# Optimization experiments

Hardware: AMD Instinct MI355X
Metric: run time of the kernel (lower is better)

Reference implementation:

```python
import jax, jax.numpy as jnp
import numpy as np

OVERFLOW_MARGIN = 1e-08

N, D, OUT = 8192, 128, 128


def setup_inputs() -> dict:
    key = jax.random.key(0)
    k1, k2, k3 = jax.random.split(key, 3)
    values = jax.random.normal(k1, (N, D), dtype=jnp.float32)
    adjacency = jax.random.uniform(k2, (N, N), dtype=jnp.float32)
    W = jax.random.normal(k3, (D, OUT), dtype=jnp.float32) * 0.05
    b = jnp.zeros((OUT,), dtype=jnp.float32)
    return {"values": values, "adjacency": adjacency, "W": W, "b": b}


def reference(values, adjacency, W, b):
    # Dense projection: fc_sc = values @ W + b  -> [N, OUT]
    fc_sc = values @ W + b
    # degree d = A @ ones -> row sums, [N]
    d = jnp.sum(adjacency, axis=1)
    d_inv_sqrt = 1.0 / (jnp.sqrt(d) + OVERFLOW_MARGIN)  # [N]
    # laplacian = diag(d_inv_sqrt) @ A @ diag(d_inv_sqrt)
    # expressed as row/col broadcast scaling (same math, no NxN diag matmuls)
    laplacian = adjacency * d_inv_sqrt[:, None] * d_inv_sqrt[None, :]
    # graph conv: [N,N] @ [N,OUT]
    return laplacian @ fc_sc
```

## Files before the change

### kernel.cpp

```cpp
#include <hip/hip_runtime.h>

#define NROWS 8192
#define DIM   128
#define RS    132

typedef __attribute__((ext_vector_type(8))) short  short8;
typedef __attribute__((ext_vector_type(4))) float  floatx4;

__device__ __forceinline__ unsigned pk_bf16(float a, float b) {
  unsigned ua = __float_as_uint(a);
  ua += 0x7fffu + ((ua >> 16) & 1u);
  unsigned ub = __float_as_uint(b);
  ub += 0x7fffu + ((ub >> 16) & 1u);
  return (ua >> 16) | (ub & 0xffff0000u);
}

__global__ __launch_bounds__(256) void k_rowsum(const float* __restrict__ A,
                                                float* __restrict__ d) {
  int w = threadIdx.x >> 6, lane = threadIdx.x & 63;
  int row = blockIdx.x * 4 + w;
  const float* ap = A + (size_t)row * NROWS + lane * 4;
  float sum = 0.f;
#pragma unroll
  for (int it = 0; it < 32; ++it) {
    float4 v = *(const float4*)(ap + (size_t)it * 256);
    sum += (v.x + v.y) + (v.z + v.w);
  }
#pragma unroll
  for (int off = 32; off; off >>= 1) sum += __shfl_down(sum, off, 64);
  if (lane == 0) d[row] = sum;
}

__global__ __launch_bounds__(256) void k_sconv(const float* __restrict__ d,
                                               float* __restrict__ s) {
  int i = blockIdx.x * 256 + threadIdx.x;
  s[i] = 1.0f / (sqrtf(d[i]) + 1e-8f);
}

__global__ __launch_bounds__(256) void k_fc(const float* __restrict__ V,
                                            const float* __restrict__ W,
                                            const float* __restrict__ b,
                                            const float* __restrict__ s,
                                            unsigned short* __restrict__ gTt) {
  __shared__ float Wl[DIM * DIM];
  __shared__ float Vl[32 * DIM];
  __shared__ unsigned short Fl[32 * DIM];
  int r0 = blockIdx.x * 32;
  {
    const float4* Wg = (const float4*)W;
    float4* Wd = (float4*)Wl;
#pragma unroll
    for (int i = 0; i < DIM * DIM / 4 / 256; ++i)
      Wd[threadIdx.x + i * 256] = Wg[threadIdx.x + i * 256];
    const float4* Vg = (const float4*)(V + (size_t)r0 * DIM);
    float4* Vd = (float4*)Vl;
#pragma unroll
    for (int i = 0; i < 32 * DIM / 4 / 256; ++i)
      Vd[threadIdx.x + i * 256] = Vg[threadIdx.x + i * 256];
  }
  __syncthreads();

  int cg = threadIdx.x & 31;
  int rg = threadIdx.x >> 5;
  float acc[4][4] = {};
  for (int dd = 0; dd < DIM; ++dd) {
    float4 w = *(const float4*)&Wl[dd * DIM + cg * 4];
#pragma unroll
    for (int rr = 0; rr < 4; ++rr) {
      float v = Vl[(rg * 4 + rr) * DIM + dd];
      acc[rr][0] += v * w.x; acc[rr][1] += v * w.y;
      acc[rr][2] += v * w.z; acc[rr][3] += v * w.w;
    }
  }
  float bb[4], sv[4];
#pragma unroll
  for (int cc = 0; cc < 4; ++cc) bb[cc] = b[cg * 4 + cc];
#pragma unroll
  for (int rr = 0; rr < 4; ++rr) sv[rr] = s[r0 + rg * 4 + rr];
#pragma unroll
  for (int rr = 0; rr < 4; ++rr)
#pragma unroll
    for (int cc = 0; cc < 4; cc += 2) {
      unsigned p = pk_bf16((acc[rr][cc]     + bb[cc])     * sv[rr],
                           (acc[rr][cc + 1] + bb[cc + 1]) * sv[rr]);
      *(unsigned*)&Fl[(rg * 4 + rr) * DIM + cg * 4 + cc] = p;
    }
  __syncthreads();

  int kblk = threadIdx.x >> 5, s5 = threadIdx.x & 31;
  int jblk = r0 >> 5;
#pragma unroll
  for (int h = 0; h < 2; ++h) {
    int L = s5 + h * 32;
    int l15 = L & 15, quad = L >> 4;
    int k = kblk * 16 + l15;
    unsigned w0 = (unsigned)Fl[(quad * 8 + 0) * DIM + k] | ((unsigned)Fl[(quad * 8 + 1) * DIM + k] << 16);
    unsigned w1 = (unsigned)Fl[(quad * 8 + 2) * DIM + k] | ((unsigned)Fl[(quad * 8 + 3) * DIM + k] << 16);
    unsigned w2 = (unsigned)Fl[(quad * 8 + 4) * DIM + k] | ((unsigned)Fl[(quad * 8 + 5) * DIM + k] << 16);
    unsigned w3 = (unsigned)Fl[(quad * 8 + 6) * DIM + k] | ((unsigned)Fl[(quad * 8 + 7) * DIM + k] << 16);
    *(uint4*)(gTt + ((size_t)(kblk * 256 + jblk) * 64 + L) * 8) = make_uint4(w0, w1, w2, w3);
  }
}

__global__ __launch_bounds__(256, 2) void k_spmm(const float* __restrict__ A,
                                                 const unsigned short* __restrict__ gTt,
                                                 const float* __restrict__ s,
                                                 float* __restrict__ out) {
  __shared__ float red[4 * 32 * RS];
  int t = threadIdx.x, w = t >> 6, lane = t & 63;
  int l15 = lane & 15, quad = lane >> 4;
  int bi = blockIdx.x;
  int jblk0 = w * 64;

  const float* ap0 = A + (size_t)(bi * 32 + l15) * NROWS + jblk0 * 32 + quad * 8;
  const float* ap1 = ap0 + (size_t)16 * NROWS;
  const unsigned short* gb = gTt + (size_t)jblk0 * 512 + lane * 8;

  floatx4 acc[8][2];
#pragma unroll
  for (int kb = 0; kb < 8; ++kb)
#pragma unroll
    for (int ib = 0; ib < 2; ++ib)
      acc[kb][ib] = (floatx4){0.f, 0.f, 0.f, 0.f};

#pragma unroll 2
  for (int it = 0; it < 64; ++it) {
    float4 a0lo = *(const float4*)(ap0);
    float4 a0hi = *(const float4*)(ap0 + 4);
    float4 a1lo = *(const float4*)(ap1);
    float4 a1hi = *(const float4*)(ap1 + 4);
    short8 gf[8];
#pragma unroll
    for (int kb = 0; kb < 8; ++kb)
      gf[kb] = *(const short8*)(gb + (size_t)kb * 256 * 512);
    union { unsigned u[4]; short8 s8; } c0, c1;
    c0.u[0] = pk_bf16(a0lo.x, a0lo.y); c0.u[1] = pk_bf16(a0lo.z, a0lo.w);
    c0.u[2] = pk_bf16(a0hi.x, a0hi.y); c0.u[3] = pk_bf16(a0hi.z, a0hi.w);
    c1.u[0] = pk_bf16(a1lo.x, a1lo.y); c1.u[1] = pk_bf16(a1lo.z, a1lo.w);
    c1.u[2] = pk_bf16(a1hi.x, a1hi.y); c1.u[3] = pk_bf16(a1hi.z, a1hi.w);
#pragma unroll
    for (int kb = 0; kb < 8; ++kb) {
      acc[kb][0] = __builtin_amdgcn_mfma_f32_16x16x32_bf16(gf[kb], c0.s8, acc[kb][0], 0, 0, 0);
      acc[kb][1] = __builtin_amdgcn_mfma_f32_16x16x32_bf16(gf[kb], c1.s8, acc[kb][1], 0, 0, 0);
    }
    ap0 += 32; ap1 += 32; gb += 512;
  }

  float* myred = red + w * 32 * RS;
#pragma unroll
  for (int ib = 0; ib < 2; ++ib)
#pragma unroll
    for (int kb = 0; kb < 8; ++kb) {
      float4 v = make_float4(acc[kb][ib][0], acc[kb][ib][1], acc[kb][ib][2], acc[kb][ib][3]);
      *(float4*)(myred + (ib * 16 + l15) * RS + kb * 16 + quad * 4) = v;
    }
  __syncthreads();

  int ii = t >> 3, kg = (t & 7) * 16;
  float4 sum[4];
#pragma unroll
  for (int c = 0; c < 4; ++c) sum[c] = make_float4(0.f, 0.f, 0.f, 0.f);
#pragma unroll
  for (int ww = 0; ww < 4; ++ww)
#pragma unroll
    for (int c = 0; c < 4; ++c) {
      float4 v = *(const float4*)(red + ww * 32 * RS + ii * RS + kg + c * 4);
      sum[c].x += v.x; sum[c].y += v.y; sum[c].z += v.z; sum[c].w += v.w;
    }
  float si = s[bi * 32 + ii];
  float* pout = out + ((size_t)(bi * 32 + ii)) * 128 + kg;
#pragma unroll
  for (int c = 0; c < 4; ++c) {
    float4 r = make_float4(si * sum[c].x, si * sum[c].y, si * sum[c].z, si * sum[c].w);
    *(float4*)(pout + c * 4) = r;
  }
}

extern "C" void kernel_launch(void* const* d_in, const int* in_sizes, int n_in,
                              void* d_out, int out_size, void* d_ws, size_t ws_size,
                              hipStream_t stream) {
  const float* values    = (const float*)d_in[0];
  const float* adjacency = (const float*)d_in[1];
  const float* W         = (const float*)d_in[2];
  const float* b         = (const float*)d_in[3];
  float* out = (float*)d_out;

  char* ws = (char*)d_ws;
  float* d            = (float*)ws;
  float* s            = (float*)(ws + 32768);
  unsigned short* gTt = (unsigned short*)(ws + 65536);

  k_rowsum<<<NROWS / 4, 256, 0, stream>>>(adjacency, d);
  k_sconv<<<NROWS / 256, 256, 0, stream>>>(d, s);
  k_fc<<<NROWS / 32, 256, 0, stream>>>(values, W, b, s, gTt);
  k_spmm<<<256, 256, 0, stream>>>(adjacency, gTt, s, out);
}
```

Measured before the change: 431.6 us.

## Fuse rsqrt into rowsum, widen SpMM split-K to 8 waves, use hardware bf16 pack

```diff
diff --git a/kernel.cpp b/kernel.cpp
--- a/kernel.cpp
+++ b/kernel.cpp
@@ -1,4 +1,5 @@
 #include <hip/hip_runtime.h>
+#include <hip/hip_bf16.h>
 
 #define NROWS 8192
 #define DIM   128
@@ -15,8 +16,13 @@
   return (ua >> 16) | (ub & 0xffff0000u);
 }
 
+__device__ __forceinline__ unsigned cvt_pk2(float lo, float hi) {
+  __hip_bfloat162 h = __float22bfloat162_rn(float2{lo, hi});
+  return *reinterpret_cast<unsigned*>(&h);
+}
+
 __global__ __launch_bounds__(256) void k_rowsum(const float* __restrict__ A,
-                                                float* __restrict__ d) {
+                                                float* __restrict__ s) {
   int w = threadIdx.x >> 6, lane = threadIdx.x & 63;
   int row = blockIdx.x * 4 + w;
   const float* ap = A + (size_t)row * NROWS + lane * 4;
@@ -28,13 +34,7 @@
   }
 #pragma unroll
   for (int off = 32; off; off >>= 1) sum += __shfl_down(sum, off, 64);
-  if (lane == 0) d[row] = sum;
-}
-
-__global__ __launch_bounds__(256) void k_sconv(const float* __restrict__ d,
-                                               float* __restrict__ s) {
-  int i = blockIdx.x * 256 + threadIdx.x;
-  s[i] = 1.0f / (sqrtf(d[i]) + 1e-8f);
+  if (lane == 0) s[row] = 1.0f / (sqrtf(sum) + 1e-8f);
 }
 
 __global__ __launch_bounds__(256) void k_fc(const float* __restrict__ V,
@@ -102,15 +102,15 @@
   }
 }
 
-__global__ __launch_bounds__(256, 2) void k_spmm(const float* __restrict__ A,
-                                                 const unsigned short* __restrict__ gTt,
-                                                 const float* __restrict__ s,
-                                                 float* __restrict__ out) {
-  __shared__ float red[4 * 32 * RS];
+__global__ __launch_bounds__(512) void k_spmm(const float* __restrict__ A,
+                                              const unsigned short* __restrict__ gTt,
+                                              const float* __restrict__ s,
+                                              float* __restrict__ out) {
+  __shared__ float red[8 * 32 * RS];
   int t = threadIdx.x, w = t >> 6, lane = t & 63;
   int l15 = lane & 15, quad = lane >> 4;
   int bi = blockIdx.x;
-  int jblk0 = w * 64;
+  int jblk0 = w * 32;
 
   const float* ap0 = A + (size_t)(bi * 32 + l15) * NROWS + jblk0 * 32 + quad * 8;
   const float* ap1 = ap0 + (size_t)16 * NROWS;
@@ -124,7 +124,7 @@
       acc[kb][ib] = (floatx4){0.f, 0.f, 0.f, 0.f};
 
 #pragma unroll 2
-  for (int it = 0; it < 64; ++it) {
+  for (int it = 0; it < 32; ++it) {
     float4 a0lo = *(const float4*)(ap0);
     float4 a0hi = *(const float4*)(ap0 + 4);
     float4 a1lo = *(const float4*)(ap1);
@@ -134,10 +134,10 @@
     for (int kb = 0; kb < 8; ++kb)
       gf[kb] = *(const short8*)(gb + (size_t)kb * 256 * 512);
     union { unsigned u[4]; short8 s8; } c0, c1;
-    c0.u[0] = pk_bf16(a0lo.x, a0lo.y); c0.u[1] = pk_bf16(a0lo.z, a0lo.w);
-    c0.u[2] = pk_bf16(a0hi.x, a0hi.y); c0.u[3] = pk_bf16(a0hi.z, a0hi.w);
-    c1.u[0] = pk_bf16(a1lo.x, a1lo.y); c1.u[1] = pk_bf16(a1lo.z, a1lo.w);
-    c1.u[2] = pk_bf16(a1hi.x, a1hi.y); c1.u[3] = pk_bf16(a1hi.z, a1hi.w);
+    c0.u[0] = cvt_pk2(a0lo.x, a0lo.y); c0.u[1] = cvt_pk2(a0lo.z, a0lo.w);
+    c0.u[2] = cvt_pk2(a0hi.x, a0hi.y); c0.u[3] = cvt_pk2(a0hi.z, a0hi.w);
+    c1.u[0] = cvt_pk2(a1lo.x, a1lo.y); c1.u[1] = cvt_pk2(a1lo.z, a1lo.w);
+    c1.u[2] = cvt_pk2(a1hi.x, a1hi.y); c1.u[3] = cvt_pk2(a1hi.z, a1hi.w);
 #pragma unroll
     for (int kb = 0; kb < 8; ++kb) {
       acc[kb][0] = __builtin_amdgcn_mfma_f32_16x16x32_bf16(gf[kb], c0.s8, acc[kb][0], 0, 0, 0);
@@ -156,24 +156,23 @@
     }
   __syncthreads();
 
-  int ii = t >> 3, kg = (t & 7) * 16;
-  float4 sum[4];
+  int ii = t >> 4, kg = (t & 15) * 8;
+  float4 sum0 = make_float4(0.f, 0.f, 0.f, 0.f);
+  float4 sum1 = make_float4(0.f, 0.f, 0.f, 0.f);
 #pragma unroll
-  for (int c = 0; c < 4; ++c) sum[c] = make_float4(0.f, 0.f, 0.f, 0.f);
-#pragma unroll
-  for (int ww = 0; ww < 4; ++ww)
-#pragma unroll
-    for (int c = 0; c < 4; ++c) {
-      float4 v = *(const float4*)(red + ww * 32 * RS + ii * RS + kg + c * 4);
-      sum[c].x += v.x; sum[c].y += v.y; sum[c].z += v.z; sum[c].w += v.w;
-    }
+  for (int ww = 0; ww < 8; ++ww) {
+    const float* rb = red + ww * 32 * RS + ii * RS + kg;
+    float4 v0 = *(const float4*)(rb);
+    float4 v1 = *(const float4*)(rb + 4);
+    sum0.x += v0.x; sum0.y += v0.y; sum0.z += v0.z; sum0.w += v0.w;
+    sum1.x += v1.x; sum1.y += v1.y; sum1.z += v1.z; sum1.w += v1.w;
+  }
   float si = s[bi * 32 + ii];
   float* pout = out + ((size_t)(bi * 32 + ii)) * 128 + kg;
-#pragma unroll
-  for (int c = 0; c < 4; ++c) {
-    float4 r = make_float4(si * sum[c].x, si * sum[c].y, si * sum[c].z, si * sum[c].w);
-    *(float4*)(pout + c * 4) = r;
-  }
+  float4 r0 = make_float4(si * sum0.x, si * sum0.y, si * sum0.z, si * sum0.w);
+  float4 r1 = make_float4(si * sum1.x, si * sum1.y, si * sum1.z, si * sum1.w);
+  *(float4*)(pout) = r0;
+  *(float4*)(pout + 4) = r1;
 }
 
 extern "C" void kernel_launch(void* const* d_in, const int* in_sizes, int n_in,
@@ -186,12 +185,10 @@
   float* out = (float*)d_out;
 
   char* ws = (char*)d_ws;
-  float* d            = (float*)ws;
-  float* s            = (float*)(ws + 32768);
-  unsigned short* gTt = (unsigned short*)(ws + 65536);
+  float* s            = (float*)ws;
+  unsigned short* gTt = (unsigned short*)(ws + 32768);
 
-  k_rowsum<<<NROWS / 4, 256, 0, stream>>>(adjacency, d);
-  k_sconv<<<NROWS / 256, 256, 0, stream>>>(d, s);
+  k_rowsum<<<NROWS / 4, 256, 0, stream>>>(adjacency, s);
   k_fc<<<NROWS / 32, 256, 0, stream>>>(values, W, b, s, gTt);
-  k_spmm<<<256, 256, 0, stream>>>(adjacency, gTt, s, out);
+  k_spmm<<<256, 512, 0, stream>>>(adjacency, gTt, s, out);
 }
```

New measurement: 434.9 us. About the same (+0.8%).
